# Kernel optimization log

Hardware: AMD Instinct MI355X
Metric: run time of the kernel (lower is better)

The kernel has to match this reference:

```python
import jax, jax.numpy as jnp
import numpy as np

FWD_TRUNCATION = 0.05
EPS_LOG = 1e-20


def setup_inputs() -> dict:
    key = jax.random.key(0)
    k1, k2, k3, k4, k5 = jax.random.split(key, 5)
    B, N, M = 32768, 1024, 64
    samples = jax.random.normal(k1, (B, M), dtype=jnp.float32)
    mask = jax.random.uniform(k2, (B, M), dtype=jnp.float32)
    centroids = jax.random.normal(k3, (N, M), dtype=jnp.float32)
    # sd kept away from 0 to avoid huge 1/sd scaling
    sd = jax.random.uniform(k4, (1, M), dtype=jnp.float32) + 0.5
    log_marginal = jax.random.normal(k5, (1, N), dtype=jnp.float32)
    return {"samples": samples, "mask": mask, "centroids": centroids,
            "sd": sd, "log_marginal": log_marginal}


def _masked_pairwise_sq_distances(A, B, mask):
    # A: [B, M] samples, B: [N, M] centroids, mask: [B, M]
    sq_mask = mask * mask
    mA = mask * A
    A_d = jnp.sum(mA * mA, axis=1, keepdims=True)            # [B, 1]
    B_d = sq_mask @ (B * B).T                                 # [B, N]
    cross = (sq_mask * A) @ B.T                                # [B, N]
    return jax.nn.relu(A_d - 2.0 * cross + B_d)               # [B, N]


def _pdf_truncate(pdf, truncation):
    # discretePdfTruncate: zero out entries below truncation * rowmax, renormalize
    threshold = truncation * jnp.max(pdf, axis=-1, keepdims=True)
    pdf = jax.nn.relu(jnp.sign(pdf - threshold)) * pdf
    return pdf / jnp.sum(pdf, axis=-1, keepdims=True)


def reference(samples, mask, centroids, sd, log_marginal):
    # Mahalanobis: fold 1/sd into the mask (sqMahalanobisDistances)
    m = mask / sd
    dist = _masked_pairwise_sq_distances(samples, centroids, m)  # [B, N]
    log_prior = jax.nn.log_softmax(log_marginal, axis=-1)        # [1, N]
    logits = log_prior - 0.5 * dist                              # [B, N]
    # softmaxWithTemperature (temperature=1) -> truncate -> renormalize
    pdf = jax.nn.softmax(logits, axis=-1)
    pdf = _pdf_truncate(pdf, FWD_TRUNCATION)
    log_pdf = jnp.log(pdf + EPS_LOG)                             # logPdfTruncate
    return pdf, log_pdf
```

## Files before the change

kernel.cpp:

```cpp
#include <hip/hip_runtime.h>
#include <math.h>

#define N_C 1024
#define M_F 64
#define B_R 32768
#define R_B 32
#define LDX 132

typedef short bf16x8 __attribute__((ext_vector_type(8)));
typedef float f32x4 __attribute__((ext_vector_type(4)));
typedef unsigned int uint4v __attribute__((ext_vector_type(4)));

__device__ __forceinline__ short f2bf(float x) {
  unsigned b = __float_as_uint(x);
  b += 0x7fffu + ((b >> 16) & 1u);
  return (short)(b >> 16);
}
__device__ __forceinline__ float bf2f(short h) {
  return __uint_as_float(((unsigned)(unsigned short)h) << 16);
}

__device__ __forceinline__ void split3(const float* f, bf16x8& h, bf16x8& m, bf16x8& l) {
  uint4v hp, mp, lp;
#pragma unroll
  for (int i = 0; i < 4; ++i) {
    const unsigned b0 = __float_as_uint(f[2 * i]);
    const unsigned b1 = __float_as_uint(f[2 * i + 1]);
    const unsigned h0 = b0 & 0xFFFF0000u, h1 = b1 & 0xFFFF0000u;
    const float r0 = f[2 * i] - __uint_as_float(h0);
    const float r1 = f[2 * i + 1] - __uint_as_float(h1);
    hp[i] = (b0 >> 16) | h1;
    const unsigned rb0 = __float_as_uint(r0), rb1 = __float_as_uint(r1);
    const unsigned m0 = rb0 & 0xFFFF0000u, m1 = rb1 & 0xFFFF0000u;
    const float s0 = r0 - __uint_as_float(m0);
    const float s1 = r1 - __uint_as_float(m1);
    mp[i] = (rb0 >> 16) | m1;
    lp[i] = (__float_as_uint(s0) >> 16) | (__float_as_uint(s1) & 0xFFFF0000u);
  }
  h = __builtin_bit_cast(bf16x8, hp);
  m = __builtin_bit_cast(bf16x8, mp);
  l = __builtin_bit_cast(bf16x8, lp);
}

__global__ void logprior_kernel(const float* __restrict__ lm, float* __restrict__ lp) {
  __shared__ float red[256];
  const int t = threadIdx.x;
  float v[4];
  float mx = -INFINITY;
#pragma unroll
  for (int i = 0; i < 4; ++i) { v[i] = lm[i * 256 + t]; mx = fmaxf(mx, v[i]); }
  red[t] = mx;
  __syncthreads();
  for (int s = 128; s > 0; s >>= 1) {
    if (t < s) red[t] = fmaxf(red[t], red[t + s]);
    __syncthreads();
  }
  mx = red[0];
  __syncthreads();
  float sum = 0.f;
#pragma unroll
  for (int i = 0; i < 4; ++i) { v[i] -= mx; sum += expf(v[i]); }
  red[t] = sum;
  __syncthreads();
  for (int s = 128; s > 0; s >>= 1) {
    if (t < s) red[t] += red[t + s];
    __syncthreads();
  }
  const float l = logf(red[0]);
#pragma unroll
  for (int i = 0; i < 4; ++i) lp[i * 256 + t] = v[i] - l;
}

__global__ void prep_y(const float* __restrict__ centroids,
                       bf16x8* __restrict__ yh, bf16x8* __restrict__ ym,
                       bf16x8* __restrict__ yl) {
  const int tid = blockIdx.x * 256 + threadIdx.x;
  const int l = tid & 63;
  const int c = (tid >> 6) & 63;
  const int s = tid >> 12;
  const int n = c * 16 + (l & 15);
  const int k0 = s * 32 + (l >> 4) * 8;
  bf16x8 h, mid, lo;
#pragma unroll
  for (int j = 0; j < 8; ++j) {
    const int k = k0 + j;
    float y;
    if (k < 64) {
      y = centroids[n * M_F + k];
    } else {
      const float cc = centroids[n * M_F + (k - 64)];
      y = cc * cc;
    }
    const short hh = f2bf(y);
    const float r1 = y - bf2f(hh);
    const short mm = f2bf(r1);
    const float r2 = r1 - bf2f(mm);
    h[j] = hh;
    mid[j] = mm;
    lo[j] = f2bf(r2);
  }
  const int blob = (s * 64 + c) * 64 + l;
  yh[blob] = h;
  ym[blob] = mid;
  yl[blob] = lo;
}

__global__ __launch_bounds__(256, 2) void rmm_main(
    const float* __restrict__ samples, const float* __restrict__ mask,
    const float* __restrict__ sd, const float* __restrict__ lp_g,
    const bf16x8* __restrict__ yh_g, const bf16x8* __restrict__ ym_g,
    const bf16x8* __restrict__ yl_g, float* __restrict__ out) {
  __shared__ float xs[R_B * LDX];
  __shared__ float lp_s[N_C];
  __shared__ float ad_s[R_B];
  __shared__ float red_s[R_B * 4];

  const int t = threadIdx.x;
  const int b0 = blockIdx.x * R_B;
  const int w = t >> 6;
  const int l = t & 63;
  const int m = l & 15;
  const int q = l >> 4;

  *(float4*)(lp_s + (t << 2)) = *(const float4*)(lp_g + (t << 2));

  {
    const int r = t >> 3;
    const int j8 = (t & 7) << 3;
    const float* sp = samples + (size_t)(b0 + r) * M_F + j8;
    const float* mp = mask + (size_t)(b0 + r) * M_F + j8;
    float sa[8], ma[8], da[8];
    *(float4*)&sa[0] = *(const float4*)sp;
    *(float4*)&sa[4] = *(const float4*)(sp + 4);
    *(float4*)&ma[0] = *(const float4*)mp;
    *(float4*)&ma[4] = *(const float4*)(mp + 4);
    *(float4*)&da[0] = *(const float4*)(sd + j8);
    *(float4*)&da[4] = *(const float4*)(sd + j8 + 4);
    float ad = 0.f;
#pragma unroll
    for (int k = 0; k < 8; ++k) {
      const float mm = ma[k] / da[k];
      const float uu = mm * mm;
      const float mA = mm * sa[k];
      ad = fmaf(mA, mA, ad);
      xs[r * LDX + j8 + k] = -2.0f * (uu * sa[k]);
      xs[r * LDX + 64 + j8 + k] = uu;
    }
#pragma unroll
    for (int off = 1; off < 8; off <<= 1) ad += __shfl_xor(ad, off, 64);
    if ((t & 7) == 0) ad_s[r] = ad;
  }

  f32x4 acc[2][16];
#pragma unroll
  for (int mt = 0; mt < 2; ++mt)
#pragma unroll
    for (int c = 0; c < 16; ++c) acc[mt][c] = (f32x4){0.f, 0.f, 0.f, 0.f};

  __syncthreads();

  const int sx[8] = {1, 2, 0, 1, 2, 0, 1, 0};
  const int sy[8] = {2, 1, 2, 1, 0, 1, 0, 0};

#pragma unroll 1
  for (int s = 0; s < 4; ++s) {
    const size_t sbase = (size_t)(s * 64 + w * 16) * 64 + l;
    const bf16x8* yh = yh_g + sbase;
    const bf16x8* ym = ym_g + sbase;
    const bf16x8* yl = yl_g + sbase;

    bf16x8 Bh[2], Bm[2], Bl[2];
#pragma unroll
    for (int p = 0; p < 2; ++p) {
      Bh[p] = yh[p * 64];
      Bm[p] = ym[p * 64];
      Bl[p] = yl[p * 64];
    }

    bf16x8 A[3][2];
#pragma unroll
    for (int mt = 0; mt < 2; ++mt) {
      const float* xp = &xs[(mt * 16 + m) * LDX + s * 32 + q * 8];
      float av[8];
      *(float4*)&av[0] = *(const float4*)xp;
      *(float4*)&av[4] = *(const float4*)(xp + 4);
      split3(av, A[0][mt], A[1][mt], A[2][mt]);
    }

#pragma unroll
    for (int c = 0; c < 16; ++c) {
      const int cur = c & 1;
      const bf16x8 bh = Bh[cur], bm = Bm[cur], bl = Bl[cur];
      if (c < 14) {
        Bh[cur] = yh[(c + 2) * 64];
        Bm[cur] = ym[(c + 2) * 64];
        Bl[cur] = yl[(c + 2) * 64];
      }
#pragma unroll
      for (int sp = 0; sp < 8; ++sp) {
        const bf16x8 bb = (sy[sp] == 0) ? bh : ((sy[sp] == 1) ? bm : bl);
#pragma unroll
        for (int mt = 0; mt < 2; ++mt)
          acc[mt][c] = __builtin_amdgcn_mfma_f32_16x16x32_bf16(
              A[sx[sp]][mt], bb, acc[mt][c], 0, 0, 0);
      }
    }
  }

  float adv[2][4];
#pragma unroll
  for (int mt = 0; mt < 2; ++mt)
#pragma unroll
    for (int g = 0; g < 4; ++g) adv[mt][g] = ad_s[mt * 16 + q * 4 + g];
  float lpv[16];
#pragma unroll
  for (int c = 0; c < 16; ++c) lpv[c] = lp_s[w * 256 + c * 16 + m];

#pragma unroll
  for (int mt = 0; mt < 2; ++mt)
#pragma unroll
    for (int c = 0; c < 16; ++c)
#pragma unroll
      for (int g = 0; g < 4; ++g) {
        const float dist = fmaxf(adv[mt][g] + acc[mt][c][g], 0.0f);
        acc[mt][c][g] = lpv[c] - 0.5f * dist;
      }

  float mx[2][4];
#pragma unroll
  for (int mt = 0; mt < 2; ++mt)
#pragma unroll
    for (int g = 0; g < 4; ++g) {
      float v = acc[mt][0][g];
#pragma unroll
      for (int c = 1; c < 16; ++c) v = fmaxf(v, acc[mt][c][g]);
#pragma unroll
      for (int off = 1; off < 16; off <<= 1) v = fmaxf(v, __shfl_xor(v, off, 64));
      mx[mt][g] = v;
    }
  if (m == 0) {
#pragma unroll
    for (int mt = 0; mt < 2; ++mt)
#pragma unroll
      for (int g = 0; g < 4; ++g) red_s[(mt * 16 + q * 4 + g) * 4 + w] = mx[mt][g];
  }
  __syncthreads();
#pragma unroll
  for (int mt = 0; mt < 2; ++mt)
#pragma unroll
    for (int g = 0; g < 4; ++g) {
      const float4 rv = *(const float4*)(&red_s[(mt * 16 + q * 4 + g) * 4]);
      mx[mt][g] = fmaxf(fmaxf(rv.x, rv.y), fmaxf(rv.z, rv.w));
    }
  __syncthreads();

  float sm[2][4];
#pragma unroll
  for (int mt = 0; mt < 2; ++mt)
#pragma unroll
    for (int g = 0; g < 4; ++g) {
      float ssum = 0.f;
#pragma unroll
      for (int c = 0; c < 16; ++c) {
        const float e = __expf(acc[mt][c][g] - mx[mt][g]);
        acc[mt][c][g] = e;
        ssum += e;
      }
#pragma unroll
      for (int off = 1; off < 16; off <<= 1) ssum += __shfl_xor(ssum, off, 64);
      sm[mt][g] = ssum;
    }
  if (m == 0) {
#pragma unroll
    for (int mt = 0; mt < 2; ++mt)
#pragma unroll
      for (int g = 0; g < 4; ++g) red_s[(mt * 16 + q * 4 + g) * 4 + w] = sm[mt][g];
  }
  __syncthreads();
#pragma unroll
  for (int mt = 0; mt < 2; ++mt)
#pragma unroll
    for (int g = 0; g < 4; ++g) {
      const float4 rv = *(const float4*)(&red_s[(mt * 16 + q * 4 + g) * 4]);
      sm[mt][g] = (rv.x + rv.y) + (rv.z + rv.w);
    }
  __syncthreads();

  float thr[2][4], qs[2][4];
#pragma unroll
  for (int mt = 0; mt < 2; ++mt)
#pragma unroll
    for (int g = 0; g < 4; ++g) {
      const float S1 = sm[mt][g];
      thr[mt][g] = 0.05f * (1.0f / S1);
      float s2 = 0.f;
#pragma unroll
      for (int c = 0; c < 16; ++c) {
        const float p = acc[mt][c][g] / S1;
        acc[mt][c][g] = p;
        s2 += (p > thr[mt][g]) ? p : 0.0f;
      }
#pragma unroll
      for (int off = 1; off < 16; off <<= 1) s2 += __shfl_xor(s2, off, 64);
      qs[mt][g] = s2;
    }
  if (m == 0) {
#pragma unroll
    for (int mt = 0; mt < 2; ++mt)
#pragma unroll
      for (int g = 0; g < 4; ++g) red_s[(mt * 16 + q * 4 + g) * 4 + w] = qs[mt][g];
  }
  __syncthreads();
#pragma unroll
  for (int mt = 0; mt < 2; ++mt)
#pragma unroll
    for (int g = 0; g < 4; ++g) {
      const float4 rv = *(const float4*)(&red_s[(mt * 16 + q * 4 + g) * 4]);
      qs[mt][g] = (rv.x + rv.y) + (rv.z + rv.w);
    }

  const size_t colbase = (size_t)(w * 256 + m);
#pragma unroll
  for (int mt = 0; mt < 2; ++mt)
#pragma unroll
    for (int g = 0; g < 4; ++g) {
      const float rq = 1.0f / qs[mt][g];
      float* orow = out + (size_t)(b0 + mt * 16 + q * 4 + g) * N_C + colbase;
      float* lrow = orow + (size_t)B_R * N_C;
#pragma unroll
      for (int c = 0; c < 16; ++c) {
        const float p = acc[mt][c][g];
        const float pf = (p > thr[mt][g]) ? (p * rq) : 0.0f;
        orow[c * 16] = pf;
        lrow[c * 16] = __logf(pf + 1e-20f);
      }
    }
}

extern "C" void kernel_launch(void* const* d_in, const int* in_sizes, int n_in,
                              void* d_out, int out_size, void* d_ws, size_t ws_size,
                              hipStream_t stream) {
  const float* samples   = (const float*)d_in[0];
  const float* mask      = (const float*)d_in[1];
  const float* centroids = (const float*)d_in[2];
  const float* sd        = (const float*)d_in[3];
  const float* lm        = (const float*)d_in[4];
  float* out = (float*)d_out;

  char* ws = (char*)d_ws;
  float* lp  = (float*)ws;
  bf16x8* yh = (bf16x8*)(ws + 4096);
  bf16x8* ym = (bf16x8*)(ws + 4096 + 262144);
  bf16x8* yl = (bf16x8*)(ws + 4096 + 2 * 262144);

  logprior_kernel<<<1, 256, 0, stream>>>(lm, lp);
  prep_y<<<64, 256, 0, stream>>>(centroids, yh, ym, yl);
  rmm_main<<<B_R / R_B, 256, 0, stream>>>(samples, mask, sd, lp, yh, ym, yl, out);
}
```

Baseline: 334.3 us.

## Halve rows per block, raise occupancy, merge prep kernels, prefetch B across stages

Shrinks the per-block row tile from 32 to 16 rows so each wave keeps a single accumulator set, and raises launch bounds to 4 blocks per CU for more latency hiding. The two small setup kernels are merged into one launch, and B-fragment prefetches now start before the sample load and carry across k-stages. The cost is that each B fragment loaded from global/L2 now feeds half as many MFMAs, so B traffic doubles.

```diff
diff --git a/kernel.cpp b/kernel.cpp
--- a/kernel.cpp
+++ b/kernel.cpp
@@ -4,7 +4,7 @@
 #define N_C 1024
 #define M_F 64
 #define B_R 32768
-#define R_B 32
+#define R_B 16
 #define LDX 132
 
 typedef short bf16x8 __attribute__((ext_vector_type(8)));
@@ -42,39 +42,42 @@
   l = __builtin_bit_cast(bf16x8, lp);
 }
 
-__global__ void logprior_kernel(const float* __restrict__ lm, float* __restrict__ lp) {
+__global__ void prep(const float* __restrict__ centroids,
+                     const float* __restrict__ lm,
+                     bf16x8* __restrict__ yh, bf16x8* __restrict__ ym,
+                     bf16x8* __restrict__ yl, float* __restrict__ lp) {
   __shared__ float red[256];
   const int t = threadIdx.x;
-  float v[4];
-  float mx = -INFINITY;
-#pragma unroll
-  for (int i = 0; i < 4; ++i) { v[i] = lm[i * 256 + t]; mx = fmaxf(mx, v[i]); }
-  red[t] = mx;
-  __syncthreads();
-  for (int s = 128; s > 0; s >>= 1) {
-    if (t < s) red[t] = fmaxf(red[t], red[t + s]);
+
+  if (blockIdx.x == 64) {
+    float v[4];
+    float mx = -INFINITY;
+#pragma unroll
+    for (int i = 0; i < 4; ++i) { v[i] = lm[i * 256 + t]; mx = fmaxf(mx, v[i]); }
+    red[t] = mx;
     __syncthreads();
-  }
-  mx = red[0];
-  __syncthreads();
-  float sum = 0.f;
-#pragma unroll
-  for (int i = 0; i < 4; ++i) { v[i] -= mx; sum += expf(v[i]); }
-  red[t] = sum;
-  __syncthreads();
-  for (int s = 128; s > 0; s >>= 1) {
-    if (t < s) red[t] += red[t + s];
+    for (int s = 128; s > 0; s >>= 1) {
+      if (t < s) red[t] = fmaxf(red[t], red[t + s]);
+      __syncthreads();
+    }
+    mx = red[0];
     __syncthreads();
-  }
-  const float l = logf(red[0]);
-#pragma unroll
-  for (int i = 0; i < 4; ++i) lp[i * 256 + t] = v[i] - l;
-}
-
-__global__ void prep_y(const float* __restrict__ centroids,
-                       bf16x8* __restrict__ yh, bf16x8* __restrict__ ym,
-                       bf16x8* __restrict__ yl) {
-  const int tid = blockIdx.x * 256 + threadIdx.x;
+    float sum = 0.f;
+#pragma unroll
+    for (int i = 0; i < 4; ++i) { v[i] -= mx; sum += expf(v[i]); }
+    red[t] = sum;
+    __syncthreads();
+    for (int s = 128; s > 0; s >>= 1) {
+      if (t < s) red[t] += red[t + s];
+      __syncthreads();
+    }
+    const float l = logf(red[0]);
+#pragma unroll
+    for (int i = 0; i < 4; ++i) lp[i * 256 + t] = v[i] - l;
+    return;
+  }
+
+  const int tid = blockIdx.x * 256 + t;
   const int l = tid & 63;
   const int c = (tid >> 6) & 63;
   const int s = tid >> 12;
@@ -105,7 +108,7 @@
   yl[blob] = lo;
 }
 
-__global__ __launch_bounds__(256, 2) void rmm_main(
+__global__ __launch_bounds__(256, 4) void rmm_main(
     const float* __restrict__ samples, const float* __restrict__ mask,
     const float* __restrict__ sd, const float* __restrict__ lp_g,
     const bf16x8* __restrict__ yh_g, const bf16x8* __restrict__ ym_g,
@@ -124,7 +127,12 @@
 
   *(float4*)(lp_s + (t << 2)) = *(const float4*)(lp_g + (t << 2));
 
-  {
+  const size_t base0 = (size_t)(w * 16) * 64 + l;
+  bf16x8 Bh[2], Bm[2], Bl[2];
+  Bh[0] = yh_g[base0];      Bm[0] = ym_g[base0];      Bl[0] = yl_g[base0];
+  Bh[1] = yh_g[base0 + 64]; Bm[1] = ym_g[base0 + 64]; Bl[1] = yl_g[base0 + 64];
+
+  if (t < 128) {
     const int r = t >> 3;
     const int j8 = (t & 7) << 3;
     const float* sp = samples + (size_t)(b0 + r) * M_F + j8;
@@ -151,11 +159,9 @@
     if ((t & 7) == 0) ad_s[r] = ad;
   }
 
-  f32x4 acc[2][16];
-#pragma unroll
-  for (int mt = 0; mt < 2; ++mt)
-#pragma unroll
-    for (int c = 0; c < 16; ++c) acc[mt][c] = (f32x4){0.f, 0.f, 0.f, 0.f};
+  f32x4 acc[16];
+#pragma unroll
+  for (int c = 0; c < 16; ++c) acc[c] = (f32x4){0.f, 0.f, 0.f, 0.f};
 
   __syncthreads();
 
@@ -169,172 +175,138 @@
     const bf16x8* ym = ym_g + sbase;
     const bf16x8* yl = yl_g + sbase;
 
-    bf16x8 Bh[2], Bm[2], Bl[2];
-#pragma unroll
-    for (int p = 0; p < 2; ++p) {
-      Bh[p] = yh[p * 64];
-      Bm[p] = ym[p * 64];
-      Bl[p] = yl[p * 64];
-    }
-
-    bf16x8 A[3][2];
-#pragma unroll
-    for (int mt = 0; mt < 2; ++mt) {
-      const float* xp = &xs[(mt * 16 + m) * LDX + s * 32 + q * 8];
+    bf16x8 A[3];
+    {
+      const float* xp = &xs[m * LDX + s * 32 + q * 8];
       float av[8];
       *(float4*)&av[0] = *(const float4*)xp;
       *(float4*)&av[4] = *(const float4*)(xp + 4);
-      split3(av, A[0][mt], A[1][mt], A[2][mt]);
+      split3(av, A[0], A[1], A[2]);
     }
 
 #pragma unroll
     for (int c = 0; c < 16; ++c) {
       const int cur = c & 1;
       const bf16x8 bh = Bh[cur], bm = Bm[cur], bl = Bl[cur];
-      if (c < 14) {
-        Bh[cur] = yh[(c + 2) * 64];
-        Bm[cur] = ym[(c + 2) * 64];
-        Bl[cur] = yl[(c + 2) * 64];
+      const int pf = c + 2;
+      if (s < 3 || pf < 16) {
+        const int off = (pf < 16) ? pf * 64 : 4096 + (pf - 16) * 64;
+        Bh[cur] = yh[off];
+        Bm[cur] = ym[off];
+        Bl[cur] = yl[off];
       }
 #pragma unroll
       for (int sp = 0; sp < 8; ++sp) {
         const bf16x8 bb = (sy[sp] == 0) ? bh : ((sy[sp] == 1) ? bm : bl);
-#pragma unroll
-        for (int mt = 0; mt < 2; ++mt)
-          acc[mt][c] = __builtin_amdgcn_mfma_f32_16x16x32_bf16(
-              A[sx[sp]][mt], bb, acc[mt][c], 0, 0, 0);
+        acc[c] = __builtin_amdgcn_mfma_f32_16x16x32_bf16(A[sx[sp]], bb, acc[c], 0, 0, 0);
       }
     }
   }
 
-  float adv[2][4];
-#pragma unroll
-  for (int mt = 0; mt < 2; ++mt)
-#pragma unroll
-    for (int g = 0; g < 4; ++g) adv[mt][g] = ad_s[mt * 16 + q * 4 + g];
+  float adv[4];
+#pragma unroll
+  for (int g = 0; g < 4; ++g) adv[g] = ad_s[q * 4 + g];
   float lpv[16];
 #pragma unroll
   for (int c = 0; c < 16; ++c) lpv[c] = lp_s[w * 256 + c * 16 + m];
 
 #pragma unroll
-  for (int mt = 0; mt < 2; ++mt)
-#pragma unroll
-    for (int c = 0; c < 16; ++c)
-#pragma unroll
-      for (int g = 0; g < 4; ++g) {
-        const float dist = fmaxf(adv[mt][g] + acc[mt][c][g], 0.0f);
-        acc[mt][c][g] = lpv[c] - 0.5f * dist;
-      }
-
-  float mx[2][4];
-#pragma unroll
-  for (int mt = 0; mt < 2; ++mt)
+  for (int c = 0; c < 16; ++c)
 #pragma unroll
     for (int g = 0; g < 4; ++g) {
-      float v = acc[mt][0][g];
-#pragma unroll
-      for (int c = 1; c < 16; ++c) v = fmaxf(v, acc[mt][c][g]);
-#pragma unroll
-      for (int off = 1; off < 16; off <<= 1) v = fmaxf(v, __shfl_xor(v, off, 64));
-      mx[mt][g] = v;
-    }
+      const float dist = fmaxf(adv[g] + acc[c][g], 0.0f);
+      acc[c][g] = lpv[c] - 0.5f * dist;
+    }
+
+  float mx[4];
+#pragma unroll
+  for (int g = 0; g < 4; ++g) {
+    float v = acc[0][g];
+#pragma unroll
+    for (int c = 1; c < 16; ++c) v = fmaxf(v, acc[c][g]);
+#pragma unroll
+    for (int off = 1; off < 16; off <<= 1) v = fmaxf(v, __shfl_xor(v, off, 64));
+    mx[g] = v;
+  }
   if (m == 0) {
 #pragma unroll
-    for (int mt = 0; mt < 2; ++mt)
-#pragma unroll
-      for (int g = 0; g < 4; ++g) red_s[(mt * 16 + q * 4 + g) * 4 + w] = mx[mt][g];
-  }
-  __syncthreads();
-#pragma unroll
-  for (int mt = 0; mt < 2; ++mt)
-#pragma unroll
-    for (int g = 0; g < 4; ++g) {
-      const float4 rv = *(const float4*)(&red_s[(mt * 16 + q * 4 + g) * 4]);
-      mx[mt][g] = fmaxf(fmaxf(rv.x, rv.y), fmaxf(rv.z, rv.w));
-    }
-  __syncthreads();
-
-  float sm[2][4];
-#pragma unroll
-  for (int mt = 0; mt < 2; ++mt)
-#pragma unroll
-    for (int g = 0; g < 4; ++g) {
-      float ssum = 0.f;
-#pragma unroll
-      for (int c = 0; c < 16; ++c) {
-        const float e = __expf(acc[mt][c][g] - mx[mt][g]);
-        acc[mt][c][g] = e;
-        ssum += e;
-      }
-#pragma unroll
-      for (int off = 1; off < 16; off <<= 1) ssum += __shfl_xor(ssum, off, 64);
-      sm[mt][g] = ssum;
-    }
+    for (int g = 0; g < 4; ++g) red_s[(q * 4 + g) * 4 + w] = mx[g];
+  }
+  __syncthreads();
+#pragma unroll
+  for (int g = 0; g < 4; ++g) {
+    const float4 rv = *(const float4*)(&red_s[(q * 4 + g) * 4]);
+    mx[g] = fmaxf(fmaxf(rv.x, rv.y), fmaxf(rv.z, rv.w));
+  }
+  __syncthreads();
+
+  float sm[4];
+#pragma unroll
+  for (int g = 0; g < 4; ++g) {
+    float ssum = 0.f;
+#pragma unroll
+    for (int c = 0; c < 16; ++c) {
+      const float e = __expf(acc[c][g] - mx[g]);
+      acc[c][g] = e;
+      ssum += e;
+    }
+#pragma unroll
+    for (int off = 1; off < 16; off <<= 1) ssum += __shfl_xor(ssum, off, 64);
+    sm[g] = ssum;
+  }
   if (m == 0) {
 #pragma unroll
-    for (int mt = 0; mt < 2; ++mt)
-#pragma unroll
-      for (int g = 0; g < 4; ++g) red_s[(mt * 16 + q * 4 + g) * 4 + w] = sm[mt][g];
-  }
-  __syncthreads();
-#pragma unroll
-  for (int mt = 0; mt < 2; ++mt)
-#pragma unroll
-    for (int g = 0; g < 4; ++g) {
-      const float4 rv = *(const float4*)(&red_s[(mt * 16 + q * 4 + g) * 4]);
-      sm[mt][g] = (rv.x + rv.y) + (rv.z + rv.w);
-    }
-  __syncthreads();
-
-  float thr[2][4], qs[2][4];
-#pragma unroll
-  for (int mt = 0; mt < 2; ++mt)
-#pragma unroll
-    for (int g = 0; g < 4; ++g) {
-      const float S1 = sm[mt][g];
-      thr[mt][g] = 0.05f * (1.0f / S1);
-      float s2 = 0.f;
-#pragma unroll
-      for (int c = 0; c < 16; ++c) {
-        const float p = acc[mt][c][g] / S1;
-        acc[mt][c][g] = p;
-        s2 += (p > thr[mt][g]) ? p : 0.0f;
-      }
-#pragma unroll
-      for (int off = 1; off < 16; off <<= 1) s2 += __shfl_xor(s2, off, 64);
-      qs[mt][g] = s2;
-    }
+    for (int g = 0; g < 4; ++g) red_s[(q * 4 + g) * 4 + w] = sm[g];
+  }
+  __syncthreads();
+#pragma unroll
+  for (int g = 0; g < 4; ++g) {
+    const float4 rv = *(const float4*)(&red_s[(q * 4 + g) * 4]);
+    sm[g] = (rv.x + rv.y) + (rv.z + rv.w);
+  }
+  __syncthreads();
+
+  float thr[4], qs[4];
+#pragma unroll
+  for (int g = 0; g < 4; ++g) {
+    const float S1 = sm[g];
+    thr[g] = 0.05f * (1.0f / S1);
+    float s2 = 0.f;
+#pragma unroll
+    for (int c = 0; c < 16; ++c) {
+      const float p = acc[c][g] / S1;
+      acc[c][g] = p;
+      s2 += (p > thr[g]) ? p : 0.0f;
+    }
+#pragma unroll
+    for (int off = 1; off < 16; off <<= 1) s2 += __shfl_xor(s2, off, 64);
+    qs[g] = s2;
+  }
   if (m == 0) {
 #pragma unroll
-    for (int mt = 0; mt < 2; ++mt)
-#pragma unroll
-      for (int g = 0; g < 4; ++g) red_s[(mt * 16 + q * 4 + g) * 4 + w] = qs[mt][g];
-  }
-  __syncthreads();
-#pragma unroll
-  for (int mt = 0; mt < 2; ++mt)
-#pragma unroll
-    for (int g = 0; g < 4; ++g) {
-      const float4 rv = *(const float4*)(&red_s[(mt * 16 + q * 4 + g) * 4]);
-      qs[mt][g] = (rv.x + rv.y) + (rv.z + rv.w);
-    }
+    for (int g = 0; g < 4; ++g) red_s[(q * 4 + g) * 4 + w] = qs[g];
+  }
+  __syncthreads();
+#pragma unroll
+  for (int g = 0; g < 4; ++g) {
+    const float4 rv = *(const float4*)(&red_s[(q * 4 + g) * 4]);
+    qs[g] = (rv.x + rv.y) + (rv.z + rv.w);
+  }
 
   const size_t colbase = (size_t)(w * 256 + m);
 #pragma unroll
-  for (int mt = 0; mt < 2; ++mt)
-#pragma unroll
-    for (int g = 0; g < 4; ++g) {
-      const float rq = 1.0f / qs[mt][g];
-      float* orow = out + (size_t)(b0 + mt * 16 + q * 4 + g) * N_C + colbase;
-      float* lrow = orow + (size_t)B_R * N_C;
-#pragma unroll
-      for (int c = 0; c < 16; ++c) {
-        const float p = acc[mt][c][g];
-        const float pf = (p > thr[mt][g]) ? (p * rq) : 0.0f;
-        orow[c * 16] = pf;
-        lrow[c * 16] = __logf(pf + 1e-20f);
-      }
-    }
+  for (int g = 0; g < 4; ++g) {
+    const float rq = 1.0f / qs[g];
+    float* orow = out + (size_t)(b0 + q * 4 + g) * N_C + colbase;
+    float* lrow = orow + (size_t)B_R * N_C;
+#pragma unroll
+    for (int c = 0; c < 16; ++c) {
+      const float p = acc[c][g];
+      const float pf = (p > thr[g]) ? (p * rq) : 0.0f;
+      orow[c * 16] = pf;
+      lrow[c * 16] = __logf(pf + 1e-20f);
+    }
+  }
 }
 
 extern "C" void kernel_launch(void* const* d_in, const int* in_sizes, int n_in,
@@ -353,7 +325,6 @@
   bf16x8* ym = (bf16x8*)(ws + 4096 + 262144);
   bf16x8* yl = (bf16x8*)(ws + 4096 + 2 * 262144);
 
-  logprior_kernel<<<1, 256, 0, stream>>>(lm, lp);
-  prep_y<<<64, 256, 0, stream>>>(centroids, yh, ym, yl);
+  prep<<<65, 256, 0, stream>>>(centroids, lm, yh, ym, yl, lp);
   rmm_main<<<B_R / R_B, 256, 0, stream>>>(samples, mask, sd, lp, yh, ym, yl, out);
 }
```

After: 349.0 us. 4.4% more time.
